# Kernel tuning notes

Measured on AMD Instinct MI355X. Metric: run time of the kernel, lower is better.

Reference implementation:

```python
import jax, jax.numpy as jnp
import numpy as np

Q, L = 512, 4096


def setup_inputs() -> dict:
    key = jax.random.key(0)
    ks = jax.random.split(key, 12)
    def rn(k, shape, s=0.05):
        return jax.random.normal(k, shape, jnp.float32) * s
    return {
        "reactions": jax.random.normal(ks[0], (1, Q, 256), jnp.float32),
        "protein":   jax.random.normal(ks[1], (1, L, 1024), jnp.float32),
        # conv1d(1024->256, k=1) == pointwise linear
        "Wc":  rn(ks[2], (256, 1024)), "bc":  jnp.zeros((256,), jnp.float32),
        "W1":  rn(ks[3], (64, 256)),   "b1":  jnp.zeros((64,), jnp.float32),
        "W2":  rn(ks[4], (64, 256)),   "b2":  jnp.zeros((64,), jnp.float32),
        "Wa":  rn(ks[5], (64, 64)),    "ba":  jnp.zeros((64,), jnp.float32),
        "Wpa": rn(ks[6], (64, 64)),    "bpa": jnp.zeros((64,), jnp.float32),
        "Wra": rn(ks[7], (64, 64)),    "bra": jnp.zeros((64,), jnp.float32),
        "Wf1": rn(ks[8], (256, 128)),  "bf1": jnp.zeros((256,), jnp.float32),
        "Wf2": rn(ks[9], (128, 256)),  "bf2": jnp.zeros((128,), jnp.float32),
        "Wf3": rn(ks[10], (1, 128)),   "bf3": jnp.zeros((1,), jnp.float32),
    }


def reference(reactions, protein, Wc, bc, W1, b1, W2, b2, Wa, ba,
              Wpa, bpa, Wra, bra, Wf1, bf1, Wf2, bf2, Wf3, bf3):
    # protein: [1, L, 1024] -> 1x1 conv over channels == linear -> [L, 256]
    p = jax.nn.relu(protein[0] @ Wc.T + bc)
    # reactions: [1, Q, 256] -> [Q, 64]
    r = jax.nn.relu(reactions[0] @ W2.T + b2)
    # protein tokens -> [L, 64]
    k = jax.nn.relu(p @ W1.T + b1)

    ra = r @ Wra.T + bra            # [Q, 64]
    pa = k @ Wpa.T + bpa            # [L, 64]
    # broadcast outer-sum + relu + small linear: [Q, L, 64]
    A = jax.nn.relu(ra[:, None, :] + pa[None, :, :]) @ Wa.T + ba

    r_gate = jax.nn.sigmoid(jnp.mean(A, axis=1))   # [Q, 64]
    p_gate = jax.nn.sigmoid(jnp.mean(A, axis=0))   # [L, 64]

    rxnfp = r + r * r_gate                          # [Q, 64]
    prot = jnp.max(k + k * p_gate, axis=0)          # [64]  maxpool over L

    ctx = jnp.concatenate(
        [rxnfp, jnp.broadcast_to(prot, (rxnfp.shape[0], 64))], axis=1)  # [Q,128]

    # dropout layers are identity in eval mode
    h = jax.nn.leaky_relu(ctx @ Wf1.T + bf1)
    h = jax.nn.leaky_relu(h @ Wf2.T + bf2)
    out = h @ Wf3.T + bf3
    return out.reshape(-1)                          # [Q]
```

## Files before the change

kernel.cpp:

```cpp
#include <hip/hip_runtime.h>
#include <hip/hip_bf16.h>
#include <math.h>

#define TPB 256

typedef __attribute__((ext_vector_type(8))) short s16x8;
typedef __attribute__((ext_vector_type(4))) float f32x4;

#define MFMA16(a, b, c) __builtin_amdgcn_mfma_f32_16x16x32_bf16((a), (b), (c), 0, 0, 0)

constexpr unsigned OFF_P    = 0u;
constexpr unsigned OFF_K    = OFF_P    + 4096u*256u;
constexpr unsigned OFF_PA   = OFF_K    + 4096u*64u;
constexpr unsigned OFF_R    = OFF_PA   + 4096u*64u;
constexpr unsigned OFF_RA   = OFF_R    + 512u*64u;
constexpr unsigned OFF_SR   = OFF_RA   + 512u*64u;
constexpr unsigned OFF_PMAX = OFF_SR   + 512u*64u;
constexpr unsigned OFF_SP   = OFF_PMAX + 64u;
constexpr unsigned OFF_PAT  = OFF_SP   + 4096u*64u;
constexpr unsigned OFF_RAT  = OFF_PAT  + 64u*4096u;

__device__ __forceinline__ short f2bf(float x) {
  union { float f; unsigned u; } v; v.f = x;
  unsigned r = v.u + 0x7FFFu + ((v.u >> 16) & 1u);
  return (short)(r >> 16);
}
__device__ __forceinline__ unsigned pkbf(float a, float b) {
  __hip_bfloat162 h = __float22bfloat162_rn(make_float2(a, b));
  union { __hip_bfloat162 h2; unsigned u; } v; v.h2 = h;
  return v.u;
}
union U8 { s16x8 s; unsigned u[4]; };

__global__ __launch_bounds__(TPB, 2) void k1_gemm(
    const float* __restrict__ prot, const float* __restrict__ Wc,
    const float* __restrict__ bc,   float* __restrict__ ws)
{
  int bid = blockIdx.x;
  int tid = threadIdx.x;
  if (bid >= 512) {
    if (tid < 16)
      *(float4*)&ws[OFF_PMAX + tid * 4] = make_float4(0.f, 0.f, 0.f, 0.f);
    return;
  }

  __shared__ __align__(16) short Asm[32 * 72];
  __shared__ __align__(16) short Bsm[64 * 72];

  int m0 = (bid >> 2) * 32;
  int n0 = (bid & 3) * 64;
  int wave = tid >> 6, lane = tid & 63;
  int wm = (wave & 1) * 16, wn = (wave >> 1) * 32;
  int lm = lane & 15, quad = lane >> 4;

  int arow = tid >> 3, aseg = (tid & 7) * 8;
  int brow = tid >> 2, bseg = (tid & 3) * 16;

  const float* Ag = prot + (size_t)(m0 + arow) * 1024 + aseg;
  const float* Bg = Wc   + (size_t)(n0 + brow) * 1024 + bseg;

  float4 a4[2], b4[4];
#pragma unroll
  for (int i = 0; i < 2; ++i) a4[i] = *(const float4*)(Ag + i * 4);
#pragma unroll
  for (int i = 0; i < 4; ++i) b4[i] = *(const float4*)(Bg + i * 4);

  f32x4 acc[2] = {};

  for (int kc = 0; kc < 16; ++kc) {
    __syncthreads();
    {
      U8 s;
      s.u[0] = pkbf(a4[0].x, a4[0].y); s.u[1] = pkbf(a4[0].z, a4[0].w);
      s.u[2] = pkbf(a4[1].x, a4[1].y); s.u[3] = pkbf(a4[1].z, a4[1].w);
      *(s16x8*)&Asm[arow * 72 + aseg] = s.s;
    }
#pragma unroll
    for (int h = 0; h < 2; ++h) {
      U8 s;
      s.u[0] = pkbf(b4[h*2].x,   b4[h*2].y);
      s.u[1] = pkbf(b4[h*2].z,   b4[h*2].w);
      s.u[2] = pkbf(b4[h*2+1].x, b4[h*2+1].y);
      s.u[3] = pkbf(b4[h*2+1].z, b4[h*2+1].w);
      *(s16x8*)&Bsm[brow * 72 + bseg + h * 8] = s.s;
    }
    if (kc < 15) {
#pragma unroll
      for (int i = 0; i < 2; ++i) a4[i] = *(const float4*)(Ag + (kc + 1) * 64 + i * 4);
#pragma unroll
      for (int i = 0; i < 4; ++i) b4[i] = *(const float4*)(Bg + (kc + 1) * 64 + i * 4);
    }
    __syncthreads();
#pragma unroll
    for (int ks = 0; ks < 2; ++ks) {
      s16x8 af = *(const s16x8*)&Asm[(wm + lm) * 72 + ks * 32 + quad * 8];
#pragma unroll
      for (int ni = 0; ni < 2; ++ni) {
        s16x8 bfv = *(const s16x8*)&Bsm[(wn + ni * 16 + lm) * 72 + ks * 32 + quad * 8];
        acc[ni] = MFMA16(af, bfv, acc[ni]);
      }
    }
  }

#pragma unroll
  for (int ni = 0; ni < 2; ++ni) {
    int col = n0 + wn + ni * 16 + lm;
    float bcv = bc[col];
#pragma unroll
    for (int r = 0; r < 4; ++r) {
      int row = m0 + wm + quad * 4 + r;
      ws[OFF_P + (unsigned)row * 256u + col] = fmaxf(acc[ni][r] + bcv, 0.f);
    }
  }
}

__global__ __launch_bounds__(TPB, 2) void k2_heads(
    const float* __restrict__ reactions,
    const float* __restrict__ W1,  const float* __restrict__ b1,
    const float* __restrict__ W2,  const float* __restrict__ b2,
    const float* __restrict__ Wpa, const float* __restrict__ bpa,
    const float* __restrict__ Wra, const float* __restrict__ bra,
    float* __restrict__ ws)
{
  __shared__ __align__(16) short Asm[32 * 264];
  __shared__ __align__(16) short Bsm[64 * 264];
  __shared__ __align__(16) short Ksm[32 * 72];
  __shared__ __align__(16) short Wsm[64 * 72];
  int bid = blockIdx.x, tid = threadIdx.x;
  bool isProt = bid < 128;
  int row0 = (isProt ? bid : (bid - 128)) * 32;
  const float* src  = isProt ? (ws + OFF_P) : reactions;
  const float* Wst1 = isProt ? W1 : W2;
  const float* bv   = isProt ? b1 : b2;
  const float* Wst2 = isProt ? Wpa : Wra;
  const float* b2nd = isProt ? bpa : bra;
  float* out1  = ws + (isProt ? OFF_K : OFF_R);
  float* out2  = ws + (isProt ? OFF_PA : OFF_RA);
  float* out2T = ws + (isProt ? OFF_PAT : OFF_RAT);
  unsigned tstride = isProt ? 4096u : 512u;

  {
    int row = tid >> 3, seg = (tid & 7) * 32;
    const float* sp = src + (size_t)(row0 + row) * 256 + seg;
    float4 f[8];
#pragma unroll
    for (int i = 0; i < 8; ++i) f[i] = *(const float4*)(sp + i * 4);
#pragma unroll
    for (int i = 0; i < 4; ++i) {
      U8 s;
      s.u[0] = pkbf(f[2*i].x,   f[2*i].y);
      s.u[1] = pkbf(f[2*i].z,   f[2*i].w);
      s.u[2] = pkbf(f[2*i+1].x, f[2*i+1].y);
      s.u[3] = pkbf(f[2*i+1].z, f[2*i+1].w);
      *(s16x8*)&Asm[row * 264 + seg + i * 8] = s.s;
    }
  }
  {
    int row = tid >> 2, seg = (tid & 3) * 64;
    const float* sp = Wst1 + (size_t)row * 256 + seg;
#pragma unroll
    for (int i = 0; i < 8; ++i) {
      float4 fa = *(const float4*)(sp + i * 8);
      float4 fb = *(const float4*)(sp + i * 8 + 4);
      U8 s;
      s.u[0] = pkbf(fa.x, fa.y); s.u[1] = pkbf(fa.z, fa.w);
      s.u[2] = pkbf(fb.x, fb.y); s.u[3] = pkbf(fb.z, fb.w);
      *(s16x8*)&Bsm[row * 264 + seg + i * 8] = s.s;
    }
  }
  {
    int row = tid >> 2, seg = (tid & 3) * 16;
    const float* sp = Wst2 + (size_t)row * 64 + seg;
#pragma unroll
    for (int i = 0; i < 2; ++i) {
      float4 fa = *(const float4*)(sp + i * 8);
      float4 fb = *(const float4*)(sp + i * 8 + 4);
      U8 s;
      s.u[0] = pkbf(fa.x, fa.y); s.u[1] = pkbf(fa.z, fa.w);
      s.u[2] = pkbf(fb.x, fb.y); s.u[3] = pkbf(fb.z, fb.w);
      *(s16x8*)&Wsm[row * 72 + seg + i * 8] = s.s;
    }
  }
  __syncthreads();

  int wave = tid >> 6, lane = tid & 63;
  int lm = lane & 15, quad = lane >> 4;
  int wm = (wave >> 1) * 16, wn = (wave & 1) * 32;

  f32x4 acc[2] = {};
#pragma unroll
  for (int kc = 0; kc < 8; ++kc) {
    s16x8 a = *(const s16x8*)&Asm[(wm + lm) * 264 + kc * 32 + quad * 8];
#pragma unroll
    for (int ni = 0; ni < 2; ++ni) {
      s16x8 b = *(const s16x8*)&Bsm[(wn + ni * 16 + lm) * 264 + kc * 32 + quad * 8];
      acc[ni] = MFMA16(a, b, acc[ni]);
    }
  }
#pragma unroll
  for (int ni = 0; ni < 2; ++ni) {
    int col = wn + ni * 16 + lm;
    float bb = bv[col];
#pragma unroll
    for (int r = 0; r < 4; ++r) {
      int row = wm + quad * 4 + r;
      float kv = fmaxf(acc[ni][r] + bb, 0.f);
      out1[(size_t)(row0 + row) * 64 + col] = kv;
      Ksm[row * 72 + col] = f2bf(kv);
    }
  }
  __syncthreads();

  f32x4 acc2[2] = {};
#pragma unroll
  for (int kc = 0; kc < 2; ++kc) {
    s16x8 a = *(const s16x8*)&Ksm[(wm + lm) * 72 + kc * 32 + quad * 8];
#pragma unroll
    for (int ni = 0; ni < 2; ++ni) {
      s16x8 b = *(const s16x8*)&Wsm[(wn + ni * 16 + lm) * 72 + kc * 32 + quad * 8];
      acc2[ni] = MFMA16(a, b, acc2[ni]);
    }
  }
#pragma unroll
  for (int ni = 0; ni < 2; ++ni) {
    int col = wn + ni * 16 + lm;
    float bb = b2nd[col];
#pragma unroll
    for (int r = 0; r < 4; ++r) {
      int row = wm + quad * 4 + r;
      float v = acc2[ni][r] + bb;
      out2[(size_t)(row0 + row) * 64 + col] = v;
      out2T[(size_t)col * tstride + (row0 + row)] = v;
    }
  }
}

__global__ __launch_bounds__(TPB) void k3h_hist(float* __restrict__ ws)
{
  __shared__ float xcol[4096];
  __shared__ float rcol[512];
  __shared__ float hc[1025];
  __shared__ float hs[1025];
  __shared__ float rmn[4], rmx[4];
  int bid = blockIdx.x, tid = threadIdx.x;
  int wave = tid >> 6, lane = tid & 63;
  bool passA = bid < 64;
  int c = passA ? bid : (bid - 64);
  const float* paT = ws + OFF_PAT + (size_t)c * 4096;
  const float* raT = ws + OFF_RAT + (size_t)c * 512;

  for (int i = tid * 4; i < 4096; i += TPB * 4)
    *(float4*)&xcol[i] = *(const float4*)(paT + i);
  if (tid * 4 < 512)
    *(float4*)&rcol[tid * 4] = *(const float4*)(raT + tid * 4);
  for (int i = tid; i < 1025; i += TPB) { hc[i] = 0.f; hs[i] = 0.f; }
  __syncthreads();

  const float* hsrc = passA ? xcol : rcol;
  int hn = passA ? 4096 : 512;
  float mn = 1e30f, mx = -1e30f;
  for (int i = tid; i < hn; i += TPB) {
    float x = hsrc[i];
    mn = fminf(mn, x); mx = fmaxf(mx, x);
  }
#pragma unroll
  for (int off = 32; off > 0; off >>= 1) {
    mn = fminf(mn, __shfl_down(mn, off));
    mx = fmaxf(mx, __shfl_down(mx, off));
  }
  if (lane == 0) { rmn[wave] = mn; rmx[wave] = mx; }
  __syncthreads();
  mn = fminf(fminf(rmn[0], rmn[1]), fminf(rmn[2], rmn[3]));
  mx = fmaxf(fmaxf(rmx[0], rmx[1]), fmaxf(rmx[2], rmx[3]));
  float w = (mx - mn) * (1.f / 1024.f);
  float invw = (w > 1e-30f) ? 1.f / w : 0.f;
  for (int i = tid; i < hn; i += TPB) {
    float x = hsrc[i];
    int b = (int)((x - mn) * invw);
    b = b < 0 ? 0 : (b > 1023 ? 1023 : b);
    atomicAdd(&hc[b], 1.f);
    atomicAdd(&hs[b], x);
  }
  __syncthreads();
  if (wave == 0) {
    float vc[16], vs[16], sc = 0.f, ss = 0.f;
#pragma unroll
    for (int i = 0; i < 16; ++i) {
      vc[i] = hc[lane * 16 + i]; sc += vc[i];
      vs[i] = hs[lane * 16 + i]; ss += vs[i];
    }
    float tc = sc, ts = ss;
#pragma unroll
    for (int off = 1; off < 64; off <<= 1) {
      float oc = __shfl_down(tc, off);
      float os = __shfl_down(ts, off);
      if (lane + off < 64) { tc += oc; ts += os; }
    }
    float runc = tc - sc, runs = ts - ss;
#pragma unroll
    for (int i = 15; i >= 0; --i) {
      runc += vc[i]; hc[lane * 16 + i] = runc;
      runs += vs[i]; hs[lane * 16 + i] = runs;
    }
  }
  __syncthreads();

  if (passA) {
    for (int q = tid; q < 512; q += TPB) {
      float u = rcol[q];
      float thr = -u;
      int b;
      if (thr < mn) b = 0;
      else { b = (int)((thr - mn) * invw) + 1; b = b > 1024 ? 1024 : b; }
      ws[OFF_SR + (unsigned)q * 64u + c] = u * hc[b] + hs[b];
// ... 129 lines not shown
#pragma unroll
    for (int r = 0; r < 4; ++r) {
      int q = quad * 4 + r;
      float v = h[nt][r] + bb;
      v = v > 0.f ? v : 0.01f * v;
      h1b[q * 264 + n] = f2bf(v);
    }
  }
  __syncthreads();

#pragma unroll 4
  for (int it = 0; it < 32; ++it) {
    int i4 = it * TPB + tid;
    int row = i4 >> 6, c4 = (i4 & 63) * 4;
    float4 v = *(const float4*)&Wf2[row * 256 + c4];
    uint2 st = make_uint2(pkbf(v.x, v.y), pkbf(v.z, v.w));
    *(uint2*)&wgt[row * 264 + c4] = st;
  }
  __syncthreads();

  f32x4 o[2] = {};
#pragma unroll
  for (int kc = 0; kc < 8; ++kc) {
    s16x8 a = *(const s16x8*)&h1b[lm * 264 + kc * 32 + quad * 8];
#pragma unroll
    for (int nt = 0; nt < 2; ++nt) {
      s16x8 b = *(const s16x8*)&wgt[(wave * 32 + nt * 16 + lm) * 264 + kc * 32 + quad * 8];
      o[nt] = MFMA16(a, b, o[nt]);
    }
  }
  float pv[4] = {0.f, 0.f, 0.f, 0.f};
#pragma unroll
  for (int nt = 0; nt < 2; ++nt) {
    int m = wave * 32 + nt * 16 + lm;
    float bb = bf2[m], w3 = Wf3[m];
#pragma unroll
    for (int r = 0; r < 4; ++r) {
      float v = o[nt][r] + bb;
      v = v > 0.f ? v : 0.01f * v;
      pv[r] += v * w3;
    }
  }
#pragma unroll
  for (int msk = 1; msk < 16; msk <<= 1)
#pragma unroll
    for (int r = 0; r < 4; ++r) pv[r] += __shfl_xor(pv[r], msk);
  if (lm == 0) {
#pragma unroll
    for (int r = 0; r < 4; ++r) red[(quad * 4 + r) * 4 + wave] = pv[r];
  }
  __syncthreads();
  if (tid < 16)
    out[q0 + tid] = red[tid * 4] + red[tid * 4 + 1] + red[tid * 4 + 2] +
                    red[tid * 4 + 3] + bf3[0];
}

extern "C" void kernel_launch(void* const* d_in, const int* in_sizes, int n_in,
                              void* d_out, int out_size, void* d_ws, size_t ws_size,
                              hipStream_t stream)
{
  const float* reactions = (const float*)d_in[0];
  const float* protein   = (const float*)d_in[1];
  const float* Wc  = (const float*)d_in[2];
  const float* bc  = (const float*)d_in[3];
  const float* W1  = (const float*)d_in[4];
  const float* b1  = (const float*)d_in[5];
  const float* W2  = (const float*)d_in[6];
  const float* b2  = (const float*)d_in[7];
  const float* Wa  = (const float*)d_in[8];
  const float* ba  = (const float*)d_in[9];
  const float* Wpa = (const float*)d_in[10];
  const float* bpa = (const float*)d_in[11];
  const float* Wra = (const float*)d_in[12];
  const float* bra = (const float*)d_in[13];
  const float* Wf1 = (const float*)d_in[14];
  const float* bf1 = (const float*)d_in[15];
  const float* Wf2 = (const float*)d_in[16];
  const float* bf2 = (const float*)d_in[17];
  const float* Wf3 = (const float*)d_in[18];
  const float* bf3 = (const float*)d_in[19];
  float* ws  = (float*)d_ws;
  float* out = (float*)d_out;

  hipLaunchKernelGGL(k1_gemm, dim3(513), dim3(TPB), 0, stream,
                     protein, Wc, bc, ws);
  hipLaunchKernelGGL(k2_heads, dim3(144), dim3(TPB), 0, stream,
                     reactions, W1, b1, W2, b2, Wpa, bpa, Wra, bra, ws);
  hipLaunchKernelGGL(k3h_hist, dim3(128), dim3(TPB), 0, stream, ws);
  hipLaunchKernelGGL(k3b_gate, dim3(256), dim3(TPB), 0, stream, Wa, ba, ws);
  hipLaunchKernelGGL(k4_final, dim3(32), dim3(TPB), 0, stream,
                     Wa, ba, Wf1, bf1, Wf2, bf2, Wf3, bf3, ws, out);
}
```

Baseline: 172.8 us.

## Fuse post-GEMM kernels into one cooperative kernel with grid syncs

Replaces the four kernels after the protein GEMM (heads, histogram, gate, final MLP) with a single cooperative kernel of 256 blocks that uses grid.sync between stages. The non-transposed pa/ra writes are dropped, since only the transposed copies are consumed. The aim is to remove the launch and inter-kernel drain gaps, which matter because each stage does little work. In exchange it adds grid-wide barriers, a 94KB shared allocation that limits occupancy, and idle blocks in stages that use fewer blocks; it falls back to the old launches if the cooperative launch fails.

After: 344.9 us. +99.6%, slower.

```diff
diff --git a/kernel.cpp b/kernel.cpp
--- a/kernel.cpp
+++ b/kernel.cpp
@@ -1,6 +1,9 @@
 #include <hip/hip_runtime.h>
+#include <hip/hip_cooperative_groups.h>
 #include <hip/hip_bf16.h>
 #include <math.h>
+
+namespace cg = cooperative_groups;
 
 #define TPB 256
 
@@ -111,6 +114,390 @@
       int row = m0 + wm + quad * 4 + r;
       ws[OFF_P + (unsigned)row * 256u + col] = fmaxf(acc[ni][r] + bcv, 0.f);
     }
+  }
+}
+
+__global__ __launch_bounds__(TPB) void kfused(
+    const float* __restrict__ reactions,
+    const float* __restrict__ W1,  const float* __restrict__ b1,
+    const float* __restrict__ W2,  const float* __restrict__ b2,
+    const float* __restrict__ Wpa, const float* __restrict__ bpa,
+    const float* __restrict__ Wra, const float* __restrict__ bra,
+    const float* __restrict__ Wa,  const float* __restrict__ ba,
+    const float* __restrict__ Wf1, const float* __restrict__ bf1,
+    const float* __restrict__ Wf2, const float* __restrict__ bf2,
+    const float* __restrict__ Wf3, const float* __restrict__ bf3,
+    float* __restrict__ ws, float* __restrict__ out)
+{
+  cg::grid_group grid = cg::this_grid();
+  __shared__ __align__(16) unsigned char SM[94208];
+  int bid = blockIdx.x, tid = threadIdx.x;
+  int wave = tid >> 6, lane = tid & 63;
+  int lm = lane & 15, quad = lane >> 4;
+
+  if (bid < 144) {
+    short* Asm = (short*)(SM);
+    short* Bsm = (short*)(SM + 16896);
+    short* Ksm = (short*)(SM + 50688);
+    short* Wsm = (short*)(SM + 55296);
+
+    bool isProt = bid < 128;
+    int row0 = (isProt ? bid : (bid - 128)) * 32;
+    const float* src  = isProt ? (ws + OFF_P) : reactions;
+    const float* Wst1 = isProt ? W1 : W2;
+    const float* bv   = isProt ? b1 : b2;
+    const float* Wst2 = isProt ? Wpa : Wra;
+    const float* b2nd = isProt ? bpa : bra;
+    float* out1  = ws + (isProt ? OFF_K : OFF_R);
+    float* out2T = ws + (isProt ? OFF_PAT : OFF_RAT);
+    unsigned tstride = isProt ? 4096u : 512u;
+
+    {
+      int row = tid >> 3, seg = (tid & 7) * 32;
+      const float* sp = src + (size_t)(row0 + row) * 256 + seg;
+      float4 f[8];
+#pragma unroll
+      for (int i = 0; i < 8; ++i) f[i] = *(const float4*)(sp + i * 4);
+#pragma unroll
+      for (int i = 0; i < 4; ++i) {
+        U8 s;
+        s.u[0] = pkbf(f[2*i].x,   f[2*i].y);
+        s.u[1] = pkbf(f[2*i].z,   f[2*i].w);
+        s.u[2] = pkbf(f[2*i+1].x, f[2*i+1].y);
+        s.u[3] = pkbf(f[2*i+1].z, f[2*i+1].w);
+        *(s16x8*)&Asm[row * 264 + seg + i * 8] = s.s;
+      }
+    }
+    {
+      int row = tid >> 2, seg = (tid & 3) * 64;
+      const float* sp = Wst1 + (size_t)row * 256 + seg;
+#pragma unroll
+      for (int i = 0; i < 8; ++i) {
+        float4 fa = *(const float4*)(sp + i * 8);
+        float4 fb = *(const float4*)(sp + i * 8 + 4);
+        U8 s;
+        s.u[0] = pkbf(fa.x, fa.y); s.u[1] = pkbf(fa.z, fa.w);
+        s.u[2] = pkbf(fb.x, fb.y); s.u[3] = pkbf(fb.z, fb.w);
+        *(s16x8*)&Bsm[row * 264 + seg + i * 8] = s.s;
+      }
+    }
+    {
+      int row = tid >> 2, seg = (tid & 3) * 16;
+      const float* sp = Wst2 + (size_t)row * 64 + seg;
+#pragma unroll
+      for (int i = 0; i < 2; ++i) {
+        float4 fa = *(const float4*)(sp + i * 8);
+        float4 fb = *(const float4*)(sp + i * 8 + 4);
+        U8 s;
+        s.u[0] = pkbf(fa.x, fa.y); s.u[1] = pkbf(fa.z, fa.w);
+        s.u[2] = pkbf(fb.x, fb.y); s.u[3] = pkbf(fb.z, fb.w);
+        *(s16x8*)&Wsm[row * 72 + seg + i * 8] = s.s;
+      }
+    }
+    __syncthreads();
+
+    int wm = (wave >> 1) * 16, wn = (wave & 1) * 32;
+
+    f32x4 acc[2] = {};
+#pragma unroll
+    for (int kc = 0; kc < 8; ++kc) {
+      s16x8 a = *(const s16x8*)&Asm[(wm + lm) * 264 + kc * 32 + quad * 8];
+#pragma unroll
+      for (int ni = 0; ni < 2; ++ni) {
+        s16x8 b = *(const s16x8*)&Bsm[(wn + ni * 16 + lm) * 264 + kc * 32 + quad * 8];
+        acc[ni] = MFMA16(a, b, acc[ni]);
+      }
+    }
+#pragma unroll
+    for (int ni = 0; ni < 2; ++ni) {
+      int col = wn + ni * 16 + lm;
+      float bb = bv[col];
+#pragma unroll
+      for (int r = 0; r < 4; ++r) {
+        int row = wm + quad * 4 + r;
+        float kv = fmaxf(acc[ni][r] + bb, 0.f);
+        out1[(size_t)(row0 + row) * 64 + col] = kv;
+        Ksm[row * 72 + col] = f2bf(kv);
+      }
+    }
+    __syncthreads();
+
+    f32x4 acc2[2] = {};
+#pragma unroll
+    for (int kc = 0; kc < 2; ++kc) {
+      s16x8 a = *(const s16x8*)&Ksm[(wm + lm) * 72 + kc * 32 + quad * 8];
+#pragma unroll
+      for (int ni = 0; ni < 2; ++ni) {
+        s16x8 b = *(const s16x8*)&Wsm[(wn + ni * 16 + lm) * 72 + kc * 32 + quad * 8];
+        acc2[ni] = MFMA16(a, b, acc2[ni]);
+      }
+    }
+#pragma unroll
+    for (int ni = 0; ni < 2; ++ni) {
+      int col = wn + ni * 16 + lm;
+      float bb = b2nd[col];
+#pragma unroll
+      for (int r = 0; r < 4; ++r) {
+        int row = wm + quad * 4 + r;
+        float v = acc2[ni][r] + bb;
+        out2T[(size_t)col * tstride + (row0 + row)] = v;
+      }
+    }
+  }
+  __threadfence();
+  grid.sync();
+
+  if (bid < 128) {
+    float* xcol = (float*)(SM);
+    float* rcol = (float*)(SM + 16384);
+    float* hc   = (float*)(SM + 18432);
+    float* hs   = (float*)(SM + 22532);
+    float* rmn  = (float*)(SM + 26632);
+    float* rmx  = (float*)(SM + 26648);
+
+    bool passA = bid < 64;
+    int c = passA ? bid : (bid - 64);
+    const float* paT = ws + OFF_PAT + (size_t)c * 4096;
+    const float* raT = ws + OFF_RAT + (size_t)c * 512;
+
+    for (int i = tid * 4; i < 4096; i += TPB * 4)
+      *(float4*)&xcol[i] = *(const float4*)(paT + i);
+    if (tid * 4 < 512)
+      *(float4*)&rcol[tid * 4] = *(const float4*)(raT + tid * 4);
+    for (int i = tid; i < 1025; i += TPB) { hc[i] = 0.f; hs[i] = 0.f; }
+    __syncthreads();
+
+    const float* hsrc = passA ? xcol : rcol;
+    int hn = passA ? 4096 : 512;
+    float mn = 1e30f, mx = -1e30f;
+    for (int i = tid; i < hn; i += TPB) {
+      float x = hsrc[i];
+      mn = fminf(mn, x); mx = fmaxf(mx, x);
+    }
+#pragma unroll
+    for (int off = 32; off > 0; off >>= 1) {
+      mn = fminf(mn, __shfl_down(mn, off));
+      mx = fmaxf(mx, __shfl_down(mx, off));
+    }
+    if (lane == 0) { rmn[wave] = mn; rmx[wave] = mx; }
+    __syncthreads();
+    mn = fminf(fminf(rmn[0], rmn[1]), fminf(rmn[2], rmn[3]));
+    mx = fmaxf(fmaxf(rmx[0], rmx[1]), fmaxf(rmx[2], rmx[3]));
+    float w = (mx - mn) * (1.f / 1024.f);
+    float invw = (w > 1e-30f) ? 1.f / w : 0.f;
+    for (int i = tid; i < hn; i += TPB) {
+      float x = hsrc[i];
+      int b = (int)((x - mn) * invw);
+      b = b < 0 ? 0 : (b > 1023 ? 1023 : b);
+      atomicAdd(&hc[b], 1.f);
+      atomicAdd(&hs[b], x);
+    }
+    __syncthreads();
+    if (wave == 0) {
+      float vc[16], vs[16], sc = 0.f, ss = 0.f;
+#pragma unroll
+      for (int i = 0; i < 16; ++i) {
+        vc[i] = hc[lane * 16 + i]; sc += vc[i];
+        vs[i] = hs[lane * 16 + i]; ss += vs[i];
+      }
+      float tc = sc, ts = ss;
+#pragma unroll
+      for (int off = 1; off < 64; off <<= 1) {
+        float oc = __shfl_down(tc, off);
+        float os = __shfl_down(ts, off);
+        if (lane + off < 64) { tc += oc; ts += os; }
+      }
+      float runc = tc - sc, runs = ts - ss;
+#pragma unroll
+      for (int i = 15; i >= 0; --i) {
+        runc += vc[i]; hc[lane * 16 + i] = runc;
+        runs += vs[i]; hs[lane * 16 + i] = runs;
+      }
+    }
+    __syncthreads();
+
+    if (passA) {
+      for (int q = tid; q < 512; q += TPB) {
+        float u = rcol[q];
+        float thr = -u;
+        int b;
+        if (thr < mn) b = 0;
+        else { b = (int)((thr - mn) * invw) + 1; b = b > 1024 ? 1024 : b; }
+        ws[OFF_SR + (unsigned)q * 64u + c] = u * hc[b] + hs[b];
+      }
+    } else {
+      for (int l = tid; l < 4096; l += TPB) {
+        float v = xcol[l];
+        float thr = -v;
+        int b;
+        if (thr < mn) b = 0;
+        else { b = (int)((thr - mn) * invw) + 1; b = b > 1024 ? 1024 : b; }
+        ws[OFF_SP + (unsigned)l * 64u + c] = v * hc[b] + hs[b];
+      }
+    }
+  }
+  __threadfence();
+  grid.sync();
+
+  {
+    float* sp  = (float*)(SM);
+    float* wat = (float*)(SM + 4096);
+    int c = tid & 63, g = tid >> 6;
+    int l0 = bid * 16;
+    {
+      int idx = tid * 4;
+      float4 v = *(const float4*)&ws[OFF_SP + (unsigned)l0 * 64u + idx];
+      v.x *= (1.f / 512.f); v.y *= (1.f / 512.f);
+      v.z *= (1.f / 512.f); v.w *= (1.f / 512.f);
+      *(float4*)&sp[idx] = v;
+    }
+    for (int it = 0; it < 16; ++it) {
+      int idx = it * TPB + tid;
+      wat[(idx & 63) * 65 + (idx >> 6)] = Wa[idx];
+    }
+    __syncthreads();
+    float vmax = 0.f;
+    float bac = ba[c];
+#pragma unroll
+    for (int i = 0; i < 4; ++i) {
+      int ll = g * 4 + i;
+      float dot = 0.f;
+#pragma unroll 8
+      for (int jj = 0; jj < 64; ++jj)
+        dot += sp[ll * 64 + jj] * wat[jj * 65 + c];
+      float pg = 1.f / (1.f + __expf(-(dot + bac)));
+      float val = ws[OFF_K + (unsigned)(l0 + ll) * 64u + c] * (1.f + pg);
+      vmax = fmaxf(vmax, val);
+    }
+    atomicMax((int*)&ws[OFF_PMAX + c], __float_as_int(vmax));
+  }
+  __threadfence();
+  grid.sync();
+
+  if (bid < 32) {
+    short* mrb  = (short*)(SM);
+    short* wab  = (short*)(SM + 2304);
+    short* ctxb = (short*)(SM + 11520);
+    short* h1b  = (short*)(SM + 15872);
+    short* wgt  = (short*)(SM + 24320);
+    float* red  = (float*)(SM + 93952);
+    int q0 = bid * 16;
+
+    {
+      int q = tid >> 4, c4 = (tid & 15) * 4;
+      float4 v = *(const float4*)&ws[OFF_SR + (unsigned)(q0 + q) * 64u + c4];
+      uint2 st = make_uint2(pkbf(v.x * (1.f/4096.f), v.y * (1.f/4096.f)),
+                            pkbf(v.z * (1.f/4096.f), v.w * (1.f/4096.f)));
+      *(uint2*)&mrb[q * 72 + c4] = st;
+    }
+#pragma unroll
+    for (int it = 0; it < 4; ++it) {
+      int i4 = it * TPB + tid;
+      int row = i4 >> 4, c4 = (i4 & 15) * 4;
+      float4 v = *(const float4*)&Wa[row * 64 + c4];
+      uint2 st = make_uint2(pkbf(v.x, v.y), pkbf(v.z, v.w));
+      *(uint2*)&wab[row * 72 + c4] = st;
+    }
+    __syncthreads();
+
+    f32x4 gacc = {};
+#pragma unroll
+    for (int kc = 0; kc < 2; ++kc) {
+      s16x8 a = *(const s16x8*)&mrb[lm * 72 + kc * 32 + quad * 8];
+      s16x8 b = *(const s16x8*)&wab[(wave * 16 + lm) * 72 + kc * 32 + quad * 8];
+      gacc = MFMA16(a, b, gacc);
+    }
+    {
+      int c = wave * 16 + lm;
+      float bac = ba[c];
+      short pb = f2bf(ws[OFF_PMAX + c]);
+#pragma unroll
+      for (int r = 0; r < 4; ++r) {
+        int q = quad * 4 + r;
+        float gg = 1.f / (1.f + __expf(-(gacc[r] + bac)));
+        float rv = ws[OFF_R + (unsigned)(q0 + q) * 64u + c];
+        ctxb[q * 136 + c]      = f2bf(rv * (1.f + gg));
+        ctxb[q * 136 + 64 + c] = pb;
+      }
+    }
+#pragma unroll 4
+    for (int it = 0; it < 32; ++it) {
+      int i4 = it * TPB + tid;
+      int row = i4 >> 5, c4 = (i4 & 31) * 4;
+      float4 v = *(const float4*)&Wf1[row * 128 + c4];
+      uint2 st = make_uint2(pkbf(v.x, v.y), pkbf(v.z, v.w));
+      *(uint2*)&wgt[row * 136 + c4] = st;
+    }
+    __syncthreads();
+
+    f32x4 h[4] = {};
+#pragma unroll
+    for (int kc = 0; kc < 4; ++kc) {
+      s16x8 a = *(const s16x8*)&ctxb[lm * 136 + kc * 32 + quad * 8];
+#pragma unroll
+      for (int nt = 0; nt < 4; ++nt) {
+        s16x8 b = *(const s16x8*)&wgt[(wave * 64 + nt * 16 + lm) * 136 + kc * 32 + quad * 8];
+        h[nt] = MFMA16(a, b, h[nt]);
+      }
+    }
+#pragma unroll
+    for (int nt = 0; nt < 4; ++nt) {
+      int n = wave * 64 + nt * 16 + lm;
+      float bb = bf1[n];
+#pragma unroll
+      for (int r = 0; r < 4; ++r) {
+        int q = quad * 4 + r;
+        float v = h[nt][r] + bb;
+        v = v > 0.f ? v : 0.01f * v;
+        h1b[q * 264 + n] = f2bf(v);
+      }
+    }
+    __syncthreads();
+
+#pragma unroll 4
+    for (int it = 0; it < 32; ++it) {
+      int i4 = it * TPB + tid;
+      int row = i4 >> 6, c4 = (i4 & 63) * 4;
+      float4 v = *(const float4*)&Wf2[row * 256 + c4];
+      uint2 st = make_uint2(pkbf(v.x, v.y), pkbf(v.z, v.w));
+      *(uint2*)&wgt[row * 264 + c4] = st;
+    }
+    __syncthreads();
+
+    f32x4 o[2] = {};
+#pragma unroll
+    for (int kc = 0; kc < 8; ++kc) {
+      s16x8 a = *(const s16x8*)&h1b[lm * 264 + kc * 32 + quad * 8];
+#pragma unroll
+      for (int nt = 0; nt < 2; ++nt) {
+        s16x8 b = *(const s16x8*)&wgt[(wave * 32 + nt * 16 + lm) * 264 + kc * 32 + quad * 8];
+        o[nt] = MFMA16(a, b, o[nt]);
+      }
+    }
+    float pv[4] = {0.f, 0.f, 0.f, 0.f};
+#pragma unroll
+    for (int nt = 0; nt < 2; ++nt) {
+      int m = wave * 32 + nt * 16 + lm;
+      float bb = bf2[m], w3 = Wf3[m];
+#pragma unroll
+      for (int r = 0; r < 4; ++r) {
+        float v = o[nt][r] + bb;
+        v = v > 0.f ? v : 0.01f * v;
+        pv[r] += v * w3;
+      }
+    }
+#pragma unroll
+    for (int msk = 1; msk < 16; msk <<= 1)
+#pragma unroll
+      for (int r = 0; r < 4; ++r) pv[r] += __shfl_xor(pv[r], msk);
+    if (lm == 0) {
+#pragma unroll
+      for (int r = 0; r < 4; ++r) red[(quad * 4 + r) * 4 + wave] = pv[r];
+    }
+    __syncthreads();
+    if (tid < 16)
+      out[q0 + tid] = red[tid * 4] + red[tid * 4 + 1] + red[tid * 4 + 2] +
+                      red[tid * 4 + 3] + bf3[0];
   }
 }
 
@@ -135,7 +522,6 @@
   const float* Wst2 = isProt ? Wpa : Wra;
   const float* b2nd = isProt ? bpa : bra;
   float* out1  = ws + (isProt ? OFF_K : OFF_R);
-  float* out2  = ws + (isProt ? OFF_PA : OFF_RA);
   float* out2T = ws + (isProt ? OFF_PAT : OFF_RAT);
   unsigned tstride = isProt ? 4096u : 512u;
 
@@ -229,7 +615,6 @@
     for (int r = 0; r < 4; ++r) {
       int row = wm + quad * 4 + r;
       float v = acc2[ni][r] + bb;
-      out2[(size_t)(row0 + row) * 64 + col] = v;
       out2T[(size_t)col * tstride + (row0 + row)] = v;
     }
   }
@@ -527,10 +912,24 @@
 
   hipLaunchKernelGGL(k1_gemm, dim3(513), dim3(TPB), 0, stream,
                      protein, Wc, bc, ws);
-  hipLaunchKernelGGL(k2_heads, dim3(144), dim3(TPB), 0, stream,
-                     reactions, W1, b1, W2, b2, Wpa, bpa, Wra, bra, ws);
-  hipLaunchKernelGGL(k3h_hist, dim3(128), dim3(TPB), 0, stream, ws);
-  hipLaunchKernelGGL(k3b_gate, dim3(256), dim3(TPB), 0, stream, Wa, ba, ws);
-  hipLaunchKernelGGL(k4_final, dim3(32), dim3(TPB), 0, stream,
-                     Wa, ba, Wf1, bf1, Wf2, bf2, Wf3, bf3, ws, out);
+
+  void* kargs[] = {
+    (void*)&reactions,
+    (void*)&W1,  (void*)&b1,  (void*)&W2,  (void*)&b2,
+    (void*)&Wpa, (void*)&bpa, (void*)&Wra, (void*)&bra,
+    (void*)&Wa,  (void*)&ba,
+    (void*)&Wf1, (void*)&bf1, (void*)&Wf2, (void*)&bf2,
+    (void*)&Wf3, (void*)&bf3,
+    (void*)&ws,  (void*)&out
+  };
+  hipError_t e = hipLaunchCooperativeKernel(kfused, dim3(256), dim3(TPB),
+                                            kargs, 0, stream);
+  if (e != hipSuccess) {
+    hipLaunchKernelGGL(k2_heads, dim3(144), dim3(TPB), 0, stream,
+                       reactions, W1, b1, W2, b2, Wpa, bpa, Wra, bra, ws);
+    hipLaunchKernelGGL(k3h_hist, dim3(128), dim3(TPB), 0, stream, ws);
+    hipLaunchKernelGGL(k3b_gate, dim3(256), dim3(TPB), 0, stream, Wa, ba, ws);
+    hipLaunchKernelGGL(k4_final, dim3(32), dim3(TPB), 0, stream,
+                       Wa, ba, Wf1, bf1, Wf2, bf2, Wf3, bf3, ws, out);
+  }
 }
```

## Pre-convert protein and Wc to bf16, enlarge GEMM tiles to 64x64x128

Applied to the files above, without the earlier changes.

Adds a separate conversion kernel that writes bf16 copies of the protein activations and Wc into workspace. The main GEMM then loads bf16 directly, using 64x64 output tiles with a 128-deep K chunk and a 2x2 MFMA block per wave, so each shared-memory fragment is reused more often. It also drops the unused row-major pa/ra store in k2_heads. The trade-off is an extra launch and an extra round trip through global memory for the bf16 copies, plus only 256 GEMM blocks, which may leave the device under-occupied.

New measurement: 170.7 us. No clear change (-1.2%).

```diff
diff --git a/kernel.cpp b/kernel.cpp
--- a/kernel.cpp
+++ b/kernel.cpp
@@ -19,6 +19,8 @@
 constexpr unsigned OFF_SP   = OFF_PMAX + 64u;
 constexpr unsigned OFF_PAT  = OFF_SP   + 4096u*64u;
 constexpr unsigned OFF_RAT  = OFF_PAT  + 64u*4096u;
+constexpr unsigned OFF_ABF  = OFF_RAT  + 64u*512u;
+constexpr unsigned OFF_WBF  = OFF_ABF  + 2097152u;
 
 __device__ __forceinline__ short f2bf(float x) {
   union { float f; unsigned u; } v; v.f = x;
@@ -32,86 +34,98 @@
 }
 union U8 { s16x8 s; unsigned u[4]; };
 
-__global__ __launch_bounds__(TPB, 2) void k1_gemm(
+__global__ __launch_bounds__(TPB) void k0_cvt(
     const float* __restrict__ prot, const float* __restrict__ Wc,
-    const float* __restrict__ bc,   float* __restrict__ ws)
-{
-  int bid = blockIdx.x;
-  int tid = threadIdx.x;
-  if (bid >= 512) {
+    float* __restrict__ ws)
+{
+  int bid = blockIdx.x, tid = threadIdx.x;
+  if (bid >= 2176) {
     if (tid < 16)
       *(float4*)&ws[OFF_PMAX + tid * 4] = make_float4(0.f, 0.f, 0.f, 0.f);
     return;
   }
-
-  __shared__ __align__(16) short Asm[32 * 72];
-  __shared__ __align__(16) short Bsm[64 * 72];
-
-  int m0 = (bid >> 2) * 32;
-  int n0 = (bid & 3) * 64;
+  const float* src; short* dst; size_t idx;
+  if (bid < 2048) {
+    src = prot; dst = (short*)(ws + OFF_ABF);
+    idx = (size_t)bid * 2048 + (size_t)tid * 8;
+  } else {
+    src = Wc;   dst = (short*)(ws + OFF_WBF);
+    idx = (size_t)(bid - 2048) * 2048 + (size_t)tid * 8;
+  }
+  float4 f0 = *(const float4*)(src + idx);
+  float4 f1 = *(const float4*)(src + idx + 4);
+  U8 s;
+  s.u[0] = pkbf(f0.x, f0.y); s.u[1] = pkbf(f0.z, f0.w);
+  s.u[2] = pkbf(f1.x, f1.y); s.u[3] = pkbf(f1.z, f1.w);
+  *(s16x8*)(dst + idx) = s.s;
+}
+
+__global__ __launch_bounds__(TPB) void k1_gemm(
+    const float* __restrict__ bc, float* __restrict__ ws)
+{
+  __shared__ __align__(16) short Asm[64 * 136];
+  __shared__ __align__(16) short Bsm[64 * 136];
+  int bid = blockIdx.x, tid = threadIdx.x;
+  int m0 = (bid >> 2) * 64, n0 = (bid & 3) * 64;
   int wave = tid >> 6, lane = tid & 63;
-  int wm = (wave & 1) * 16, wn = (wave >> 1) * 32;
   int lm = lane & 15, quad = lane >> 4;
-
-  int arow = tid >> 3, aseg = (tid & 7) * 8;
-  int brow = tid >> 2, bseg = (tid & 3) * 16;
-
-  const float* Ag = prot + (size_t)(m0 + arow) * 1024 + aseg;
-  const float* Bg = Wc   + (size_t)(n0 + brow) * 1024 + bseg;
-
-  float4 a4[2], b4[4];
-#pragma unroll
-  for (int i = 0; i < 2; ++i) a4[i] = *(const float4*)(Ag + i * 4);
-#pragma unroll
-  for (int i = 0; i < 4; ++i) b4[i] = *(const float4*)(Bg + i * 4);
-
-  f32x4 acc[2] = {};
-
-  for (int kc = 0; kc < 16; ++kc) {
+  int wm = (wave & 1) * 32, wn = (wave >> 1) * 32;
+
+  const short* Abf = (const short*)(ws + OFF_ABF);
+  const short* Wbf = (const short*)(ws + OFF_WBF);
+  int srow = tid >> 2, sc = (tid & 3) * 32;
+  const short* Ag = Abf + (size_t)(m0 + srow) * 1024 + sc;
+  const short* Bg = Wbf + (size_t)(n0 + srow) * 1024 + sc;
+
+  s16x8 ar[4], br[4];
+#pragma unroll
+  for (int i = 0; i < 4; ++i) {
+    ar[i] = *(const s16x8*)(Ag + i * 8);
+    br[i] = *(const s16x8*)(Bg + i * 8);
+  }
+
+  f32x4 acc[2][2] = {};
+
+  for (int kc = 0; kc < 8; ++kc) {
     __syncthreads();
-    {
-      U8 s;
-      s.u[0] = pkbf(a4[0].x, a4[0].y); s.u[1] = pkbf(a4[0].z, a4[0].w);
-      s.u[2] = pkbf(a4[1].x, a4[1].y); s.u[3] = pkbf(a4[1].z, a4[1].w);
-      *(s16x8*)&Asm[arow * 72 + aseg] = s.s;
-    }
-#pragma unroll
-    for (int h = 0; h < 2; ++h) {
-      U8 s;
-      s.u[0] = pkbf(b4[h*2].x,   b4[h*2].y);
-      s.u[1] = pkbf(b4[h*2].z,   b4[h*2].w);
-      s.u[2] = pkbf(b4[h*2+1].x, b4[h*2+1].y);
-      s.u[3] = pkbf(b4[h*2+1].z, b4[h*2+1].w);
-      *(s16x8*)&Bsm[brow * 72 + bseg + h * 8] = s.s;
-    }
-    if (kc < 15) {
-#pragma unroll
-      for (int i = 0; i < 2; ++i) a4[i] = *(const float4*)(Ag + (kc + 1) * 64 + i * 4);
-#pragma unroll
-      for (int i = 0; i < 4; ++i) b4[i] = *(const float4*)(Bg + (kc + 1) * 64 + i * 4);
+#pragma unroll
+    for (int i = 0; i < 4; ++i) {
+      *(s16x8*)&Asm[srow * 136 + sc + i * 8] = ar[i];
+      *(s16x8*)&Bsm[srow * 136 + sc + i * 8] = br[i];
+    }
+    if (kc < 7) {
+#pragma unroll
+      for (int i = 0; i < 4; ++i) {
+        ar[i] = *(const s16x8*)(Ag + (kc + 1) * 128 + i * 8);
+        br[i] = *(const s16x8*)(Bg + (kc + 1) * 128 + i * 8);
+      }
     }
     __syncthreads();
 #pragma unroll
-    for (int ks = 0; ks < 2; ++ks) {
-      s16x8 af = *(const s16x8*)&Asm[(wm + lm) * 72 + ks * 32 + quad * 8];
-#pragma unroll
-      for (int ni = 0; ni < 2; ++ni) {
-        s16x8 bfv = *(const s16x8*)&Bsm[(wn + ni * 16 + lm) * 72 + ks * 32 + quad * 8];
-        acc[ni] = MFMA16(af, bfv, acc[ni]);
+    for (int ks = 0; ks < 4; ++ks) {
+      s16x8 a0 = *(const s16x8*)&Asm[(wm + lm)      * 136 + ks * 32 + quad * 8];
+      s16x8 a1 = *(const s16x8*)&Asm[(wm + 16 + lm) * 136 + ks * 32 + quad * 8];
+      s16x8 b0 = *(const s16x8*)&Bsm[(wn + lm)      * 136 + ks * 32 + quad * 8];
+      s16x8 b1 = *(const s16x8*)&Bsm[(wn + 16 + lm) * 136 + ks * 32 + quad * 8];
+      acc[0][0] = MFMA16(a0, b0, acc[0][0]);
+      acc[0][1] = MFMA16(a0, b1, acc[0][1]);
+      acc[1][0] = MFMA16(a1, b0, acc[1][0]);
+      acc[1][1] = MFMA16(a1, b1, acc[1][1]);
+    }
+  }
+
+#pragma unroll
+  for (int mi = 0; mi < 2; ++mi)
+#pragma unroll
+    for (int ni = 0; ni < 2; ++ni) {
+      int col = n0 + wn + ni * 16 + lm;
+      float bcv = bc[col];
+#pragma unroll
+      for (int r = 0; r < 4; ++r) {
+        int row = m0 + wm + mi * 16 + quad * 4 + r;
+        ws[OFF_P + (unsigned)row * 256u + col] = fmaxf(acc[mi][ni][r] + bcv, 0.f);
       }
     }
-  }
-
-#pragma unroll
-  for (int ni = 0; ni < 2; ++ni) {
-    int col = n0 + wn + ni * 16 + lm;
-    float bcv = bc[col];
-#pragma unroll
-    for (int r = 0; r < 4; ++r) {
-      int row = m0 + wm + quad * 4 + r;
-      ws[OFF_P + (unsigned)row * 256u + col] = fmaxf(acc[ni][r] + bcv, 0.f);
-    }
-  }
 }
 
 __global__ __launch_bounds__(TPB, 2) void k2_heads(
@@ -135,7 +149,6 @@
   const float* Wst2 = isProt ? Wpa : Wra;
   const float* b2nd = isProt ? bpa : bra;
   float* out1  = ws + (isProt ? OFF_K : OFF_R);
-  float* out2  = ws + (isProt ? OFF_PA : OFF_RA);
   float* out2T = ws + (isProt ? OFF_PAT : OFF_RAT);
   unsigned tstride = isProt ? 4096u : 512u;
 
@@ -229,7 +242,6 @@
     for (int r = 0; r < 4; ++r) {
       int row = wm + quad * 4 + r;
       float v = acc2[ni][r] + bb;
-      out2[(size_t)(row0 + row) * 64 + col] = v;
       out2T[(size_t)col * tstride + (row0 + row)] = v;
     }
   }
@@ -525,8 +537,10 @@
   float* ws  = (float*)d_ws;
   float* out = (float*)d_out;
 
-  hipLaunchKernelGGL(k1_gemm, dim3(513), dim3(TPB), 0, stream,
-                     protein, Wc, bc, ws);
+  hipLaunchKernelGGL(k0_cvt, dim3(2177), dim3(TPB), 0, stream,
+                     protein, Wc, ws);
+  hipLaunchKernelGGL(k1_gemm, dim3(256), dim3(TPB), 0, stream,
+                     bc, ws);
   hipLaunchKernelGGL(k2_heads, dim3(144), dim3(TPB), 0, stream,
                      reactions, W1, b1, W2, b2, Wpa, bpa, Wra, bra, ws);
   hipLaunchKernelGGL(k3h_hist, dim3(128), dim3(TPB), 0, stream, ws);
```

## Fuse protein conv GEMM with projection heads, keeping conv output in LDS

Applied to the files above, without the earlier changes.

Merges the 1x1 conv GEMM kernel with the heads kernel so each block computes a full 32x256 ReLU(conv) tile into shared memory and immediately applies W1 and Wpa. This removes the global write and re-read of the intermediate P buffer and one kernel launch, and drops the unused non-transposed PA/RA stores. In exchange the conv GEMM runs on 128 large blocks instead of 512 small ones, using about 64KB LDS and more registers, which lowers parallelism and latency hiding.

New measurement: 193.4 us. 1.12x slower.

```diff
diff --git a/kernel.cpp b/kernel.cpp
--- a/kernel.cpp
+++ b/kernel.cpp
@@ -9,12 +9,9 @@
 
 #define MFMA16(a, b, c) __builtin_amdgcn_mfma_f32_16x16x32_bf16((a), (b), (c), 0, 0, 0)
 
-constexpr unsigned OFF_P    = 0u;
-constexpr unsigned OFF_K    = OFF_P    + 4096u*256u;
-constexpr unsigned OFF_PA   = OFF_K    + 4096u*64u;
-constexpr unsigned OFF_R    = OFF_PA   + 4096u*64u;
-constexpr unsigned OFF_RA   = OFF_R    + 512u*64u;
-constexpr unsigned OFF_SR   = OFF_RA   + 512u*64u;
+constexpr unsigned OFF_K    = 0u;
+constexpr unsigned OFF_R    = OFF_K    + 4096u*64u;
+constexpr unsigned OFF_SR   = OFF_R    + 512u*64u;
 constexpr unsigned OFF_PMAX = OFF_SR   + 512u*64u;
 constexpr unsigned OFF_SP   = OFF_PMAX + 64u;
 constexpr unsigned OFF_PAT  = OFF_SP   + 4096u*64u;
@@ -32,89 +29,9 @@
 }
 union U8 { s16x8 s; unsigned u[4]; };
 
-__global__ __launch_bounds__(TPB, 2) void k1_gemm(
+__global__ __launch_bounds__(TPB) void kA_fused(
     const float* __restrict__ prot, const float* __restrict__ Wc,
-    const float* __restrict__ bc,   float* __restrict__ ws)
-{
-  int bid = blockIdx.x;
-  int tid = threadIdx.x;
-  if (bid >= 512) {
-    if (tid < 16)
-      *(float4*)&ws[OFF_PMAX + tid * 4] = make_float4(0.f, 0.f, 0.f, 0.f);
-    return;
-  }
-
-  __shared__ __align__(16) short Asm[32 * 72];
-  __shared__ __align__(16) short Bsm[64 * 72];
-
-  int m0 = (bid >> 2) * 32;
-  int n0 = (bid & 3) * 64;
-  int wave = tid >> 6, lane = tid & 63;
-  int wm = (wave & 1) * 16, wn = (wave >> 1) * 32;
-  int lm = lane & 15, quad = lane >> 4;
-
-  int arow = tid >> 3, aseg = (tid & 7) * 8;
-  int brow = tid >> 2, bseg = (tid & 3) * 16;
-
-  const float* Ag = prot + (size_t)(m0 + arow) * 1024 + aseg;
-  const float* Bg = Wc   + (size_t)(n0 + brow) * 1024 + bseg;
-
-  float4 a4[2], b4[4];
-#pragma unroll
-  for (int i = 0; i < 2; ++i) a4[i] = *(const float4*)(Ag + i * 4);
-#pragma unroll
-  for (int i = 0; i < 4; ++i) b4[i] = *(const float4*)(Bg + i * 4);
-
-  f32x4 acc[2] = {};
-
-  for (int kc = 0; kc < 16; ++kc) {
-    __syncthreads();
-    {
-      U8 s;
-      s.u[0] = pkbf(a4[0].x, a4[0].y); s.u[1] = pkbf(a4[0].z, a4[0].w);
-      s.u[2] = pkbf(a4[1].x, a4[1].y); s.u[3] = pkbf(a4[1].z, a4[1].w);
-      *(s16x8*)&Asm[arow * 72 + aseg] = s.s;
-    }
-#pragma unroll
-    for (int h = 0; h < 2; ++h) {
-      U8 s;
-      s.u[0] = pkbf(b4[h*2].x,   b4[h*2].y);
-      s.u[1] = pkbf(b4[h*2].z,   b4[h*2].w);
-      s.u[2] = pkbf(b4[h*2+1].x, b4[h*2+1].y);
-      s.u[3] = pkbf(b4[h*2+1].z, b4[h*2+1].w);
-      *(s16x8*)&Bsm[brow * 72 + bseg + h * 8] = s.s;
-    }
-    if (kc < 15) {
-#pragma unroll
-      for (int i = 0; i < 2; ++i) a4[i] = *(const float4*)(Ag + (kc + 1) * 64 + i * 4);
-#pragma unroll
-      for (int i = 0; i < 4; ++i) b4[i] = *(const float4*)(Bg + (kc + 1) * 64 + i * 4);
-    }
-    __syncthreads();
-#pragma unroll
-    for (int ks = 0; ks < 2; ++ks) {
-      s16x8 af = *(const s16x8*)&Asm[(wm + lm) * 72 + ks * 32 + quad * 8];
-#pragma unroll
-      for (int ni = 0; ni < 2; ++ni) {
-        s16x8 bfv = *(const s16x8*)&Bsm[(wn + ni * 16 + lm) * 72 + ks * 32 + quad * 8];
-        acc[ni] = MFMA16(af, bfv, acc[ni]);
-      }
-    }
-  }
-
-#pragma unroll
-  for (int ni = 0; ni < 2; ++ni) {
-    int col = n0 + wn + ni * 16 + lm;
-    float bcv = bc[col];
-#pragma unroll
-    for (int r = 0; r < 4; ++r) {
-      int row = m0 + wm + quad * 4 + r;
-      ws[OFF_P + (unsigned)row * 256u + col] = fmaxf(acc[ni][r] + bcv, 0.f);
-    }
-  }
-}
-
-__global__ __launch_bounds__(TPB, 2) void k2_heads(
+    const float* __restrict__ bc,
     const float* __restrict__ reactions,
     const float* __restrict__ W1,  const float* __restrict__ b1,
     const float* __restrict__ W2,  const float* __restrict__ b2,
@@ -122,26 +39,85 @@
     const float* __restrict__ Wra, const float* __restrict__ bra,
     float* __restrict__ ws)
 {
-  __shared__ __align__(16) short Asm[32 * 264];
-  __shared__ __align__(16) short Bsm[64 * 264];
-  __shared__ __align__(16) short Ksm[32 * 72];
-  __shared__ __align__(16) short Wsm[64 * 72];
   int bid = blockIdx.x, tid = threadIdx.x;
+  if (bid >= 144) {
+    if (tid < 16)
+      *(float4*)&ws[OFF_PMAX + tid * 4] = make_float4(0.f, 0.f, 0.f, 0.f);
+    return;
+  }
+  __shared__ __align__(16) unsigned char SM[64512];
+  short* Psm  = (short*)(SM);
+  short* Asm0 = (short*)(SM + 16896);
+  short* Bsm0 = (short*)(SM + 21504);
+  short* BsmW = (short*)(SM + 16896);
+  short* Wsm  = (short*)(SM + 50688);
+  short* Ksm  = (short*)(SM + 59904);
+
+  int wave = tid >> 6, lane = tid & 63;
+  int lm = lane & 15, quad = lane >> 4;
   bool isProt = bid < 128;
   int row0 = (isProt ? bid : (bid - 128)) * 32;
-  const float* src  = isProt ? (ws + OFF_P) : reactions;
-  const float* Wst1 = isProt ? W1 : W2;
-  const float* bv   = isProt ? b1 : b2;
-  const float* Wst2 = isProt ? Wpa : Wra;
-  const float* b2nd = isProt ? bpa : bra;
-  float* out1  = ws + (isProt ? OFF_K : OFF_R);
-  float* out2  = ws + (isProt ? OFF_PA : OFF_RA);
-  float* out2T = ws + (isProt ? OFF_PAT : OFF_RAT);
-  unsigned tstride = isProt ? 4096u : 512u;
-
-  {
+
+  if (isProt) {
+    int arow = tid >> 3, aseg = (tid & 7) * 8;
+    const float* Ag = prot + (size_t)(row0 + arow) * 1024 + aseg;
+    const float* Bg = Wc + (size_t)tid * 1024;
+    int wm = (wave & 1) * 16, wn = (wave >> 1) * 128;
+
+    float4 a4[2], b4[16];
+#pragma unroll
+    for (int i = 0; i < 2; ++i) a4[i] = *(const float4*)(Ag + i * 4);
+#pragma unroll
+    for (int i = 0; i < 16; ++i) b4[i] = *(const float4*)(Bg + i * 4);
+
+    f32x4 acc0[8] = {};
+    for (int kc = 0; kc < 16; ++kc) {
+      __syncthreads();
+      {
+        U8 s;
+        s.u[0] = pkbf(a4[0].x, a4[0].y); s.u[1] = pkbf(a4[0].z, a4[0].w);
+        s.u[2] = pkbf(a4[1].x, a4[1].y); s.u[3] = pkbf(a4[1].z, a4[1].w);
+        *(s16x8*)&Asm0[arow * 72 + aseg] = s.s;
+      }
+#pragma unroll
+      for (int h = 0; h < 8; ++h) {
+        U8 s;
+        s.u[0] = pkbf(b4[2*h].x,   b4[2*h].y);
+        s.u[1] = pkbf(b4[2*h].z,   b4[2*h].w);
+        s.u[2] = pkbf(b4[2*h+1].x, b4[2*h+1].y);
+        s.u[3] = pkbf(b4[2*h+1].z, b4[2*h+1].w);
+        *(s16x8*)&Bsm0[tid * 72 + h * 8] = s.s;
+      }
+      if (kc < 15) {
+#pragma unroll
+        for (int i = 0; i < 2; ++i) a4[i] = *(const float4*)(Ag + (kc + 1) * 64 + i * 4);
+#pragma unroll
+        for (int i = 0; i < 16; ++i) b4[i] = *(const float4*)(Bg + (kc + 1) * 64 + i * 4);
+      }
+      __syncthreads();
+#pragma unroll
+      for (int ks = 0; ks < 2; ++ks) {
+        s16x8 a = *(const s16x8*)&Asm0[(wm + lm) * 72 + ks * 32 + quad * 8];
+#pragma unroll
+        for (int nf = 0; nf < 8; ++nf) {
+          s16x8 b = *(const s16x8*)&Bsm0[(wn + nf * 16 + lm) * 72 + ks * 32 + quad * 8];
+          acc0[nf] = MFMA16(a, b, acc0[nf]);
+        }
+      }
+    }
+#pragma unroll
+    for (int nf = 0; nf < 8; ++nf) {
+      int col = wn + nf * 16 + lm;
+      float bcv = bc[col];
+#pragma unroll
+      for (int r = 0; r < 4; ++r) {
+        int row = wm + quad * 4 + r;
+        Psm[row * 264 + col] = f2bf(fmaxf(acc0[nf][r] + bcv, 0.f));
+      }
+    }
+  } else {
     int row = tid >> 3, seg = (tid & 7) * 32;
-    const float* sp = src + (size_t)(row0 + row) * 256 + seg;
+    const float* sp = reactions + (size_t)(row0 + row) * 256 + seg;
     float4 f[8];
 #pragma unroll
     for (int i = 0; i < 8; ++i) f[i] = *(const float4*)(sp + i * 4);
@@ -152,9 +128,19 @@
       s.u[1] = pkbf(f[2*i].z,   f[2*i].w);
       s.u[2] = pkbf(f[2*i+1].x, f[2*i+1].y);
       s.u[3] = pkbf(f[2*i+1].z, f[2*i+1].w);
-      *(s16x8*)&Asm[row * 264 + seg + i * 8] = s.s;
-    }
-  }
+      *(s16x8*)&Psm[row * 264 + seg + i * 8] = s.s;
+    }
+  }
+  __syncthreads();
+
+  const float* Wst1 = isProt ? W1 : W2;
+  const float* bv   = isProt ? b1 : b2;
+  const float* Wst2 = isProt ? Wpa : Wra;
+  const float* b2nd = isProt ? bpa : bra;
+  float* out1  = ws + (isProt ? OFF_K : OFF_R);
+  float* out2T = ws + (isProt ? OFF_PAT : OFF_RAT);
+  unsigned tstride = isProt ? 4096u : 512u;
+
   {
     int row = tid >> 2, seg = (tid & 3) * 64;
     const float* sp = Wst1 + (size_t)row * 256 + seg;
@@ -165,7 +151,7 @@
       U8 s;
       s.u[0] = pkbf(fa.x, fa.y); s.u[1] = pkbf(fa.z, fa.w);
       s.u[2] = pkbf(fb.x, fb.y); s.u[3] = pkbf(fb.z, fb.w);
-      *(s16x8*)&Bsm[row * 264 + seg + i * 8] = s.s;
+      *(s16x8*)&BsmW[row * 264 + seg + i * 8] = s.s;
     }
   }
   {
@@ -183,27 +169,24 @@
   }
   __syncthreads();
 
-  int wave = tid >> 6, lane = tid & 63;
-  int lm = lane & 15, quad = lane >> 4;
-  int wm = (wave >> 1) * 16, wn = (wave & 1) * 32;
-
+  int wm1 = (wave >> 1) * 16, wn1 = (wave & 1) * 32;
   f32x4 acc[2] = {};
 #pragma unroll
   for (int kc = 0; kc < 8; ++kc) {
-    s16x8 a = *(const s16x8*)&Asm[(wm + lm) * 264 + kc * 32 + quad * 8];
+    s16x8 a = *(const s16x8*)&Psm[(wm1 + lm) * 264 + kc * 32 + quad * 8];
 #pragma unroll
     for (int ni = 0; ni < 2; ++ni) {
-      s16x8 b = *(const s16x8*)&Bsm[(wn + ni * 16 + lm) * 264 + kc * 32 + quad * 8];
+      s16x8 b = *(const s16x8*)&BsmW[(wn1 + ni * 16 + lm) * 264 + kc * 32 + quad * 8];
       acc[ni] = MFMA16(a, b, acc[ni]);
     }
   }
 #pragma unroll
   for (int ni = 0; ni < 2; ++ni) {
-    int col = wn + ni * 16 + lm;
+    int col = wn1 + ni * 16 + lm;
     float bb = bv[col];
 #pragma unroll
     for (int r = 0; r < 4; ++r) {
-      int row = wm + quad * 4 + r;
+      int row = wm1 + quad * 4 + r;
       float kv = fmaxf(acc[ni][r] + bb, 0.f);
       out1[(size_t)(row0 + row) * 64 + col] = kv;
       Ksm[row * 72 + col] = f2bf(kv);
@@ -214,22 +197,21 @@
   f32x4 acc2[2] = {};
 #pragma unroll
   for (int kc = 0; kc < 2; ++kc) {
-    s16x8 a = *(const s16x8*)&Ksm[(wm + lm) * 72 + kc * 32 + quad * 8];
+    s16x8 a = *(const s16x8*)&Ksm[(wm1 + lm) * 72 + kc * 32 + quad * 8];
 #pragma unroll
     for (int ni = 0; ni < 2; ++ni) {
-      s16x8 b = *(const s16x8*)&Wsm[(wn + ni * 16 + lm) * 72 + kc * 32 + quad * 8];
+      s16x8 b = *(const s16x8*)&Wsm[(wn1 + ni * 16 + lm) * 72 + kc * 32 + quad * 8];
       acc2[ni] = MFMA16(a, b, acc2[ni]);
     }
   }
 #pragma unroll
   for (int ni = 0; ni < 2; ++ni) {
-    int col = wn + ni * 16 + lm;
+    int col = wn1 + ni * 16 + lm;
     float bb = b2nd[col];
 #pragma unroll
     for (int r = 0; r < 4; ++r) {
-      int row = wm + quad * 4 + r;
+      int row = wm1 + quad * 4 + r;
       float v = acc2[ni][r] + bb;
-      out2[(size_t)(row0 + row) * 64 + col] = v;
       out2T[(size_t)col * tstride + (row0 + row)] = v;
     }
   }
@@ -525,10 +507,9 @@
   float* ws  = (float*)d_ws;
   float* out = (float*)d_out;
 
-  hipLaunchKernelGGL(k1_gemm, dim3(513), dim3(TPB), 0, stream,
-                     protein, Wc, bc, ws);
-  hipLaunchKernelGGL(k2_heads, dim3(144), dim3(TPB), 0, stream,
-                     reactions, W1, b1, W2, b2, Wpa, bpa, Wra, bra, ws);
+  hipLaunchKernelGGL(kA_fused, dim3(145), dim3(TPB), 0, stream,
+                     protein, Wc, bc, reactions,
+                     W1, b1, W2, b2, Wpa, bpa, Wra, bra, ws);
   hipLaunchKernelGGL(k3h_hist, dim3(128), dim3(TPB), 0, stream, ws);
   hipLaunchKernelGGL(k3b_gate, dim3(256), dim3(TPB), 0, stream, Wa, ba, ws);
   hipLaunchKernelGGL(k4_final, dim3(32), dim3(TPB), 0, stream,
```
